# Kernel optimization log

Measured on AMD Instinct MI355X. Metric: run time of the kernel, lower is better.

The kernel has to match this reference:

```python
import jax, jax.numpy as jnp
import numpy as np

B, N, F, H, M, EF, OUT = 256, 32, 40, 100, 100, 4, 128
MESSAGE_PASSES = 3


def setup_inputs() -> dict:
    key = jax.random.key(0)
    ks = jax.random.split(key, 8)
    # Deterministic ring graphs: node i <-> node (i+1)%N, one-hot bond type.
    # Every node has degree 2 -> static nonzero counts.
    rng = np.random.default_rng(0)
    edges = np.zeros((B, N, N, EF), np.float32)
    b = np.arange(B)[:, None]
    i = np.arange(N)[None, :]
    j = (i + 1) % N
    t = rng.integers(0, EF, size=(B, N))
    edges[b, i, j, t] = 1.0
    edges[b, j, i, t] = 1.0

    nodes = jax.random.normal(ks[0], (B, N, F), jnp.float32)

    def init(k, shape, fan):
        return jax.random.normal(k, shape, jnp.float32) / np.sqrt(fan).astype(np.float32)

    W_msg = init(ks[1], (M, H, EF), H)          # MNN edge-conditioned weights
    W_ih = init(ks[2], (3 * H, M), M)            # GRUCell input weights
    W_hh = init(ks[3], (3 * H, H), H)            # GRUCell hidden weights
    b_ih = jnp.zeros((3 * H,), jnp.float32)
    b_hh = jnp.zeros((3 * H,), jnp.float32)
    Wg = init(ks[4], (H + F, H), H + F)          # gather gate
    bg = jnp.zeros((H,), jnp.float32)
    We = init(ks[5], (H, H), H)                  # gather embed
    be = jnp.zeros((H,), jnp.float32)
    Wo = init(ks[6], (H, OUT), H)                # output head
    bo = jnp.zeros((OUT,), jnp.float32)

    return {
        "nodes": nodes, "edges": jnp.asarray(edges),
        "W_msg": W_msg, "W_ih": W_ih, "W_hh": W_hh, "b_ih": b_ih, "b_hh": b_hh,
        "Wg": Wg, "bg": bg, "We": We, "be": be, "Wo": Wo, "bo": bo,
        "n_edges": B * N * 2, "n_node_entries": B * N,
    }


def gru_cell(x, h, W_ih, W_hh, b_ih, b_hh):
    gi = x @ W_ih.T + b_ih
    gh = h @ W_hh.T + b_hh
    ir, iz, inn = jnp.split(gi, 3, axis=-1)
    hr, hz, hn = jnp.split(gh, 3, axis=-1)
    r = jax.nn.sigmoid(ir + hr)
    z = jax.nn.sigmoid(iz + hz)
    n = jnp.tanh(inn + r * hn)
    return (1.0 - z) * n + z * h


def reference(nodes, edges, W_msg, W_ih, W_hh, b_ih, b_hh, Wg, bg, We, be, Wo, bo,
              n_edges, n_node_entries):
    adjacency = jnp.sum(edges, axis=3)                      # (B, N, N)
    eb, en, eg = jnp.nonzero(adjacency, size=n_edges)       # edge-level indices
    nb, nn_ = jnp.nonzero(adjacency.sum(-1), size=n_node_entries)

    # Dense one-hot segment-sum matrix: (n_node_entries, n_edges)
    same = (nb[:, None] == eb) & (nn_[:, None] == en)
    msg_sum_mat = same.astype(jnp.float32)

    edge_batch_edges = edges[eb, en, eg, :]                 # (E, EF)

    hidden = jnp.zeros((B, N, H), jnp.float32).at[:, :, :F].set(nodes)
    node_h = hidden[nb, nn_, :]                             # (V, H)

    for _ in range(MESSAGE_PASSES):
        nghb_h = hidden[eb, eg, :]                          # (E, H)
        # MNN message: sum_f edges[e,f] * W_msg[m,h,f] * nghb[e,h]
        message_terms = jnp.einsum('ef,mhf,eh->em', edge_batch_edges, W_msg, nghb_h)
        messages = msg_sum_mat @ message_terms              # (V, M) dense one-hot matmul
        node_h = gru_cell(messages, node_h, W_ih, W_hh, b_ih, b_hh)
        hidden = hidden.at[nb, nn_, :].set(node_h)

    node_mask = (adjacency.sum(-1) != 0).astype(jnp.float32)  # (B, N)
    cat = jnp.concatenate([hidden, nodes], axis=-1)           # (B, N, H+F)
    gate = jax.nn.sigmoid(cat @ Wg + bg)
    emb = gate * (hidden @ We + be)
    graph_emb = jnp.sum(emb * node_mask[..., None], axis=1)   # (B, H)
    return graph_emb @ Wo + bo                                # (B, OUT)
```

## Files before the change

### kernel.cpp

```cpp
#include <hip/hip_runtime.h>
#include <cstddef>
#include <cstdint>

#define B_   256
#define N_   32
#define F_   40
#define H_   100
#define OUT_ 128
#define CAP_ 8
#define TB   1024
#define XCS  168
#define XMS  136
#define NBLK 343
#define NLO  63

using bf16x8 = __attribute__((ext_vector_type(8))) short;
using f32x4  = __attribute__((ext_vector_type(4))) float;

__device__ __forceinline__ float sigmoidf_(float x){ return 1.0f/(1.0f+__expf(-x)); }
__device__ __forceinline__ float bf2f(short s){ return __uint_as_float(((uint32_t)(uint16_t)s)<<16); }
__device__ __forceinline__ short f2bf(float x){
  uint32_t u = __float_as_uint(x);
  return (short)((u + 0x7FFFu + ((u>>16)&1u))>>16);
}
__device__ __forceinline__ void bsplit(float x, short& hi, short& lo){
  hi = f2bf(x);
  lo = f2bf(x - bf2f(hi));
}

__global__ void prep_frags2(const float* __restrict__ Wmsg,
                            const float* __restrict__ Wih,
                            const float* __restrict__ Whh,
                            const float* __restrict__ Wg,
                            const float* __restrict__ We,
                            short* __restrict__ AFhi,
                            short* __restrict__ AFlo){
  int i = blockIdx.x*blockDim.x + threadIdx.x;
  if (i < 40000){
    float v = Wmsg[i];
    int t = i&3, mk = i>>2, h = mk%100, m = mk/100;
    int blk = t*28 + (m>>4)*4 + (h>>5);
    int lane = (m&15) + (((h&31)>>3)<<4);
    AFhi[(size_t)blk*512 + lane*8 + (h&7)] = f2bf(v);
  } else if (i < 70000){
    int i2 = i-40000;
    float v = Wih[i2];
    int jrow = i2/100, k = i2%100, mat = jrow/100, mg = jrow%100;
    int blk = 112 + mat*28 + (mg>>4)*4 + (k>>5);
    int lane = (mg&15) + (((k&31)>>3)<<4);
    AFhi[(size_t)blk*512 + lane*8 + (k&7)] = f2bf(v);
  } else if (i < 100000){
    int i2 = i-70000;
    float v = Whh[i2];
    int jrow = i2/100, k = i2%100, mat = 3 + jrow/100, mg = jrow%100;
    int blk = 112 + mat*28 + (mg>>4)*4 + (k>>5);
    int lane = (mg&15) + (((k&31)>>3)<<4);
    AFhi[(size_t)blk*512 + lane*8 + (k&7)] = f2bf(v);
  } else if (i < 114000){
    int i2 = i-100000;
    float v = Wg[i2];
    int k = i2/100, j = i2%100;
    int blk = 280 + (j>>4)*5 + (k>>5);
    int lane = (j&15) + (((k&31)>>3)<<4);
    short hi,lo; bsplit(v,hi,lo);
    AFhi[(size_t)blk*512 + lane*8 + (k&7)] = hi;
    AFlo[(size_t)(blk-280)*512 + lane*8 + (k&7)] = lo;
  } else if (i < 124000){
    int i2 = i-114000;
    float v = We[i2];
    int k = i2/100, j = i2%100;
    int blk = 315 + (j>>4)*4 + (k>>5);
    int lane = (j&15) + (((k&31)>>3)<<4);
    short hi,lo; bsplit(v,hi,lo);
    AFhi[(size_t)blk*512 + lane*8 + (k&7)] = hi;
    AFlo[(size_t)(blk-280)*512 + lane*8 + (k&7)] = lo;
  }
}

__device__ __forceinline__ bf16x8 ldB(const short* X, int stride, int nt, int ks, int lane){
  int n = nt*16 + (lane&15);
  return *(const bf16x8*)&X[n*stride + ks*32 + (lane>>4)*8];
}
__device__ __forceinline__ bf16x8 ldA(const short* __restrict__ AF, int blk, int lane){
  return *(const bf16x8*)(AF + (size_t)blk*512 + lane*8);
}

__global__ __launch_bounds__(TB, 4) void mpnn_mfma(
    const float* __restrict__ nodes, const float* __restrict__ edges,
    const short* __restrict__ AFhi, const short* __restrict__ AFlo,
    const float* __restrict__ b_ih, const float* __restrict__ b_hh,
    const float* __restrict__ bg, const float* __restrict__ be,
    const float* __restrict__ Wo, const float* __restrict__ bo,
    float* __restrict__ out){
  const int b = blockIdx.x;
  const int tid = threadIdx.x;
  const int lane = tid & 63;
  const int w = tid >> 6;

  __shared__ short XcH[32*XCS], XcL[32*XCS];
  __shared__ short XmH[32*XMS];
  __shared__ short XyH[4][32*XMS];
  __shared__ float sh_ge[H_];
  __shared__ float sh_part[4][OUT_];
  __shared__ float sh_rowsum[N_];
  __shared__ int   sh_cnt[N_];
  __shared__ int   sh_gt[N_][CAP_];
  __shared__ float sh_w[N_][CAP_];

  for (int i=tid;i<(32*XCS)/2;i+=TB){ ((int*)XcH)[i]=0; ((int*)XcL)[i]=0; }
  for (int i=tid;i<(32*XMS)/2;i+=TB){ ((int*)XmH)[i]=0; }
  if (tid < H_) sh_ge[tid]=0.0f;
  if (tid < N_){ sh_cnt[tid]=0; sh_rowsum[tid]=0.0f; }
  __syncthreads();

  for (int p=tid; p<N_*N_; p+=TB){
    int n = p>>5, g = p&31;
    const float4 ev = *(const float4*)(edges + (((size_t)b*N_+n)*N_+g)*4);
    float adj = ev.x+ev.y+ev.z+ev.w;
    if (adj != 0.0f){
      atomicAdd(&sh_rowsum[n], adj);
      float ef[4] = {ev.x,ev.y,ev.z,ev.w};
      for (int f=0; f<4; ++f)
        if (ef[f] != 0.0f){
          int s = atomicAdd(&sh_cnt[n],1);
          if (s<CAP_){ sh_gt[n][s]=(g<<2)|f; sh_w[n][s]=ef[f]; }
        }
    }
  }
  for (int p=tid; p<N_*F_; p+=TB){
    int n = p/F_, f = p%F_;
    float x = nodes[((size_t)b*N_+n)*F_ + f];
    short hi,lo; bsplit(x,hi,lo);
    XcH[n*XCS+f]=hi;      XcL[n*XCS+f]=lo;
    XcH[n*XCS+100+f]=hi;  XcL[n*XCS+100+f]=lo;
  }
  __syncthreads();

  const int jmt = w>>1, nt = w&1;
  const bool task = (w < 14);

  for (int pass=0; pass<3; ++pass){
    for (int it=0; it<2; ++it){
      int idx = tid + it*TB;
      int n = idx >> 6;
      int kp = idx & 63;
      int cnt = sh_cnt[n] < CAP_ ? sh_cnt[n] : CAP_;
      float s0[4]={0,0,0,0}, s1[4]={0,0,0,0};
      for (int e=0;e<cnt;++e){
        int gt = sh_gt[n][e];
        int g = gt>>2; float wv = sh_w[n][e];
        int hh = ((const int*)(XcH + g*XCS))[kp];
        float h0 = bf2f((short)(hh&0xffff));
        float h1 = bf2f((short)(hh>>16));
        int t = gt&3;
        if (t==0)      { s0[0]+=wv*h0; s1[0]+=wv*h1; }
        else if (t==1) { s0[1]+=wv*h0; s1[1]+=wv*h1; }
        else if (t==2) { s0[2]+=wv*h0; s1[2]+=wv*h1; }
        else           { s0[3]+=wv*h0; s1[3]+=wv*h1; }
      }
#pragma unroll
      for (int t=0;t<4;++t){
        ((int*)(XyH[t] + n*XMS))[kp] =
          (int)((uint16_t)f2bf(s0[t]) | ((uint32_t)(uint16_t)f2bf(s1[t])<<16));
      }
    }
    __syncthreads();
    f32x4 Ch0=(f32x4)0.0f, Ch1=(f32x4)0.0f, Ch2=(f32x4)0.0f;
    if (task){
      f32x4 Cm0=(f32x4)0.0f, Cm1=(f32x4)0.0f;
      {
        bf16x8 ah = ldA(AFhi, jmt*4, lane);
        bf16x8 bh = ldB(XyH[0],XMS,nt,0,lane);
#pragma unroll 1
        for (int i=0;i<16;++i){
          int ip = (i<15)? i+1 : 15;
          int tp = ip>>2, ksp = ip&3;
          bf16x8 an  = ldA(AFhi, tp*28+jmt*4+ksp, lane);
          bf16x8 bhn = ldB(XyH[tp],XMS,nt,ksp,lane);
          if (i<8) Cm0 = __builtin_amdgcn_mfma_f32_16x16x32_bf16(ah, bh, Cm0, 0,0,0);
          else     Cm1 = __builtin_amdgcn_mfma_f32_16x16x32_bf16(ah, bh, Cm1, 0,0,0);
          ah = an; bh = bhn;
        }
      }
      {
        bf16x8 ah = ldA(AFhi, 112+3*28+jmt*4, lane);
        bf16x8 bh = ldB(XcH,XCS,nt,0,lane);
#pragma unroll 1
        for (int i=0;i<12;++i){
          int ip = (i<11)? i+1 : 11;
          int gp = ip>>2, ksp = ip&3;
          bf16x8 an  = ldA(AFhi, 112+(gp+3)*28+jmt*4+ksp, lane);
          bf16x8 bhn = ldB(XcH,XCS,nt,ksp,lane);
          int g = i>>2;
          if (g==0)      Ch0 = __builtin_amdgcn_mfma_f32_16x16x32_bf16(ah, bh, Ch0, 0,0,0);
          else if (g==1) Ch1 = __builtin_amdgcn_mfma_f32_16x16x32_bf16(ah, bh, Ch1, 0,0,0);
          else           Ch2 = __builtin_amdgcn_mfma_f32_16x16x32_bf16(ah, bh, Ch2, 0,0,0);
          ah = an; bh = bhn;
        }
      }
      f32x4 Cm = Cm0 + Cm1;
      int n = nt*16+(lane&15);
      for (int r=0;r<4;++r){
        int row = jmt*16 + (lane>>4)*4 + r;
        if (row<100) XmH[n*XMS+row] = f2bf(Cm[r]);
      }
    }
    __syncthreads();
    if (task){
      f32x4 Ci0=(f32x4)0.0f, Ci1=(f32x4)0.0f, Ci2=(f32x4)0.0f;
      {
        bf16x8 ah = ldA(AFhi, 112+jmt*4, lane);
        bf16x8 bh = ldB(XmH,XMS,nt,0,lane);
#pragma unroll 1
        for (int i=0;i<12;++i){
          int ip = (i<11)? i+1 : 11;
          int gp = ip>>2, ksp = ip&3;
          bf16x8 an  = ldA(AFhi, 112+gp*28+jmt*4+ksp, lane);
          bf16x8 bhn = ldB(XmH,XMS,nt,ksp,lane);
          int g = i>>2;
          if (g==0)      Ci0 = __builtin_amdgcn_mfma_f32_16x16x32_bf16(ah, bh, Ci0, 0,0,0);
          else if (g==1) Ci1 = __builtin_amdgcn_mfma_f32_16x16x32_bf16(ah, bh, Ci1, 0,0,0);
          else           Ci2 = __builtin_amdgcn_mfma_f32_16x16x32_bf16(ah, bh, Ci2, 0,0,0);
          ah = an; bh = bhn;
        }
      }
      int n = nt*16+(lane&15);
      bool msk = (sh_rowsum[n] != 0.0f);
      for (int r=0;r<4;++r){
        int row = jmt*16 + (lane>>4)*4 + r;
        if (row<100){
          float ho = bf2f(XcH[n*XCS+row]) + bf2f(XcL[n*XCS+row]);
          float rr = sigmoidf_(Ci0[r]+Ch0[r] + b_ih[row]     + b_hh[row]);
          float zz = sigmoidf_(Ci1[r]+Ch1[r] + b_ih[100+row] + b_hh[100+row]);
          float nn = tanhf(Ci2[r] + b_ih[200+row] + rr*(Ch2[r] + b_hh[200+row]));
          float hnew = (1.0f-zz)*nn + zz*ho;
          if (!msk) hnew = ho;
          short hi,lo; bsplit(hnew,hi,lo);
          XcH[n*XCS+row]=hi; XcL[n*XCS+row]=lo;
        }
      }
    }
    __syncthreads();
  }

  f32x4 Cg=(f32x4)0.0f, Ce=(f32x4)0.0f;
  if (task){
    bf16x8 ah = ldA(AFhi, 280+jmt*5, lane);
    bf16x8 al = ldA(AFlo, jmt*5, lane);
    bf16x8 bh = ldB(XcH,XCS,nt,0,lane);
#pragma unroll 1
    for (int i=0;i<9;++i){
      int ip = (i<8)? i+1 : 8;
      int blkp  = (ip<5)? 280+jmt*5+ip : 315+jmt*4+(ip-5);
      int ksp   = (ip<5)? ip : ip-5;
      bf16x8 an  = ldA(AFhi, blkp, lane);
      bf16x8 aln = ldA(AFlo, blkp-280, lane);
      bf16x8 bhn = ldB(XcH,XCS,nt,ksp,lane);
      if (i<5){
        Cg = __builtin_amdgcn_mfma_f32_16x16x32_bf16(ah, bh, Cg, 0,0,0);
        Cg = __builtin_amdgcn_mfma_f32_16x16x32_bf16(al, bh, Cg, 0,0,0);
      } else {
        Ce = __builtin_amdgcn_mfma_f32_16x16x32_bf16(ah, bh, Ce, 0,0,0);
        Ce = __builtin_amdgcn_mfma_f32_16x16x32_bf16(al, bh, Ce, 0,0,0);
      }
      ah = an; al = aln; bh = bhn;
    }
    int n = nt*16+(lane&15);
    bool msk = (sh_rowsum[n] != 0.0f);
    for (int r=0;r<4;++r){
      int row = jmt*16 + (lane>>4)*4 + r;
      float v = 0.0f;
      if (row<100){
        float gate = sigmoidf_(Cg[r] + bg[row]);
        float emb  = gate*(Ce[r] + be[row]);
        v = msk ? emb : 0.0f;
      }
      v += __shfl_xor(v, 1);
      v += __shfl_xor(v, 2);
      v += __shfl_xor(v, 4);
      v += __shfl_xor(v, 8);
      if (row<100 && (lane&15)==0) atomicAdd(&sh_ge[row], v);
    }
  }
  __syncthreads();
  if (tid < 512){
    int o = tid & 127, q = tid >> 7;
    float s = 0.0f;
    int k0 = 25*q;
#pragma unroll 5
    for (int k=k0; k<k0+25; ++k) s += sh_ge[k]*Wo[k*OUT_+o];
    sh_part[q][o] = s;
  }
  __syncthreads();
  if (tid < OUT_){
    out[(size_t)b*OUT_ + tid] = bo[tid] + sh_part[0][tid] + sh_part[1][tid]
                              + sh_part[2][tid] + sh_part[3][tid];
  }
}

extern "C" void kernel_launch(void* const* d_in, const int* in_sizes, int n_in,
                              void* d_out, int out_size, void* d_ws, size_t ws_size,
                              hipStream_t stream){
  const float* nodes = (const float*)d_in[0];
  const float* edges = (const float*)d_in[1];
  const float* W_msg = (const float*)d_in[2];
  const float* W_ih  = (const float*)d_in[3];
  const float* W_hh  = (const float*)d_in[4];
  const float* b_ih  = (const float*)d_in[5];
  const float* b_hh  = (const float*)d_in[6];
  const float* Wg    = (const float*)d_in[7];
  const float* bg    = (const float*)d_in[8];
  const float* We    = (const float*)d_in[9];
  const float* be    = (const float*)d_in[10];
  const float* Wo    = (const float*)d_in[11];
  const float* bo    = (const float*)d_in[12];

  short* AFhi = (short*)d_ws;
  short* AFlo = AFhi + (size_t)NBLK*512;
  size_t af_bytes = ((size_t)NBLK + NLO) * 512 * sizeof(short);

  hipMemsetAsync(d_ws, 0, af_bytes, stream);
  prep_frags2<<<(124000 + 255)/256, 256, 0, stream>>>(W_msg, W_ih, W_hh, Wg, We,
                                                      AFhi, AFlo);
  mpnn_mfma<<<B_, TB, 0, stream>>>(nodes, edges, AFhi, AFlo, b_ih, b_hh, bg, be,
                                   Wo, bo, (float*)d_out);
}
```

Measured before the change: 133.9 us.

## Fold message weights into GRU input weights and use MFMA for neighbor aggregation

Precomputes W_ih·W_msg per edge type in the prep kernel, so the message matmul and the GRU input matmul collapse into one 48-step MFMA chain. This removes one stage and one barrier per pass. Neighbor aggregation moves from a per-edge list loop to a dense adjacency-by-hidden MFMA over a transposed hidden copy. The hidden state is double-buffered, tanh uses a fast exp form, and the memset is dropped because the prep kernel now writes every slot. In exchange it does more MFMA work on the dense 32x32 adjacency, and folding the weights changes where bf16 rounding happens.

New measurement: 153.9 us. 15.0% more time.

```diff
diff --git a/kernel.cpp b/kernel.cpp
--- a/kernel.cpp
+++ b/kernel.cpp
@@ -7,17 +7,21 @@
 #define F_   40
 #define H_   100
 #define OUT_ 128
-#define CAP_ 8
 #define TB   1024
 #define XCS  168
 #define XMS  136
-#define NBLK 343
+#define ST2  40
+#define NBLK 483
 #define NLO  63
 
 using bf16x8 = __attribute__((ext_vector_type(8))) short;
 using f32x4  = __attribute__((ext_vector_type(4))) float;
 
 __device__ __forceinline__ float sigmoidf_(float x){ return 1.0f/(1.0f+__expf(-x)); }
+__device__ __forceinline__ float tanhf_(float x){
+  float e = __expf(2.0f*x);
+  return 1.0f - 2.0f/(e+1.0f);
+}
 __device__ __forceinline__ float bf2f(short s){ return __uint_as_float(((uint32_t)(uint16_t)s)<<16); }
 __device__ __forceinline__ short f2bf(float x){
   uint32_t u = __float_as_uint(x);
@@ -28,52 +32,48 @@
   lo = f2bf(x - bf2f(hi));
 }
 
-__global__ void prep_frags2(const float* __restrict__ Wmsg,
+__global__ void prep_frags3(const float* __restrict__ Wmsg,
                             const float* __restrict__ Wih,
                             const float* __restrict__ Whh,
                             const float* __restrict__ Wg,
                             const float* __restrict__ We,
                             short* __restrict__ AFhi,
                             short* __restrict__ AFlo){
-  int i = blockIdx.x*blockDim.x + threadIdx.x;
-  if (i < 40000){
-    float v = Wmsg[i];
-    int t = i&3, mk = i>>2, h = mk%100, m = mk/100;
-    int blk = t*28 + (m>>4)*4 + (h>>5);
-    int lane = (m&15) + (((h&31)>>3)<<4);
-    AFhi[(size_t)blk*512 + lane*8 + (h&7)] = f2bf(v);
-  } else if (i < 70000){
-    int i2 = i-40000;
-    float v = Wih[i2];
-    int jrow = i2/100, k = i2%100, mat = jrow/100, mg = jrow%100;
-    int blk = 112 + mat*28 + (mg>>4)*4 + (k>>5);
-    int lane = (mg&15) + (((k&31)>>3)<<4);
-    AFhi[(size_t)blk*512 + lane*8 + (k&7)] = f2bf(v);
-  } else if (i < 100000){
-    int i2 = i-70000;
-    float v = Whh[i2];
-    int jrow = i2/100, k = i2%100, mat = 3 + jrow/100, mg = jrow%100;
-    int blk = 112 + mat*28 + (mg>>4)*4 + (k>>5);
-    int lane = (mg&15) + (((k&31)>>3)<<4);
-    AFhi[(size_t)blk*512 + lane*8 + (k&7)] = f2bf(v);
-  } else if (i < 114000){
-    int i2 = i-100000;
-    float v = Wg[i2];
-    int k = i2/100, j = i2%100;
-    int blk = 280 + (j>>4)*5 + (k>>5);
-    int lane = (j&15) + (((k&31)>>3)<<4);
+  int slot = blockIdx.x*blockDim.x + threadIdx.x;
+  if (slot >= NBLK*512) return;
+  int blk = slot>>9, r = slot&511, lane = r>>3, jj = r&7;
+  int m = lane&15, q = lane>>4, kl = q*8+jj;
+  if (blk < 336){
+    int sub = blk/28, rem = blk%28;
+    int g = sub>>2, t = sub&3, jmt = rem>>2, ks = rem&3;
+    int jo = jmt*16+m, h = ks*32+kl;
+    float v = 0.0f;
+    if (jo<100 && h<100){
+      const float* wr = Wih + (g*100+jo)*100;
+      const float* wc = Wmsg + h*4 + t;
+#pragma unroll 4
+      for (int m2=0;m2<100;++m2) v += wr[m2]*wc[m2*400];
+    }
+    AFhi[slot] = f2bf(v);
+  } else if (blk < 420){
+    int bb = blk-336, mat = bb/28, rem = bb%28, jmt = rem>>2, ks = rem&3;
+    int jo = jmt*16+m, k = ks*32+kl;
+    float v = (jo<100 && k<100) ? Whh[(mat*100+jo)*100+k] : 0.0f;
+    AFhi[slot] = f2bf(v);
+  } else if (blk < 455){
+    int bb = blk-420, jmt = bb/5, ks = bb%5;
+    int jo = jmt*16+m, k = ks*32+kl;
+    float v = (jo<100 && k<140) ? Wg[k*100+jo] : 0.0f;
     short hi,lo; bsplit(v,hi,lo);
-    AFhi[(size_t)blk*512 + lane*8 + (k&7)] = hi;
-    AFlo[(size_t)(blk-280)*512 + lane*8 + (k&7)] = lo;
-  } else if (i < 124000){
-    int i2 = i-114000;
-    float v = We[i2];
-    int k = i2/100, j = i2%100;
-    int blk = 315 + (j>>4)*4 + (k>>5);
-    int lane = (j&15) + (((k&31)>>3)<<4);
+    AFhi[slot] = hi;
+    AFlo[(size_t)(blk-420)*512 + lane*8 + jj] = lo;
+  } else {
+    int bb = blk-455, jmt = bb>>2, ks = bb&3;
+    int jo = jmt*16+m, k = ks*32+kl;
+    float v = (jo<100 && k<100) ? We[k*100+jo] : 0.0f;
     short hi,lo; bsplit(v,hi,lo);
-    AFhi[(size_t)blk*512 + lane*8 + (k&7)] = hi;
-    AFlo[(size_t)(blk-280)*512 + lane*8 + (k&7)] = lo;
+    AFhi[slot] = hi;
+    AFlo[(size_t)(blk-420)*512 + lane*8 + jj] = lo;
   }
 }
 
@@ -97,100 +97,94 @@
   const int lane = tid & 63;
   const int w = tid >> 6;
 
-  __shared__ short XcH[32*XCS], XcL[32*XCS];
-  __shared__ short XmH[32*XMS];
-  __shared__ short XyH[4][32*XMS];
+  __shared__ short XcH[2][32*XCS];
+  __shared__ short XcL[32*XCS];
+  __shared__ short XcT[2][112*ST2];
+  __shared__ short XyH[4*32*XMS];
+  __shared__ short Aw[4*32*32];
   __shared__ float sh_ge[H_];
   __shared__ float sh_part[4][OUT_];
   __shared__ float sh_rowsum[N_];
-  __shared__ int   sh_cnt[N_];
-  __shared__ int   sh_gt[N_][CAP_];
-  __shared__ float sh_w[N_][CAP_];
-
-  for (int i=tid;i<(32*XCS)/2;i+=TB){ ((int*)XcH)[i]=0; ((int*)XcL)[i]=0; }
-  for (int i=tid;i<(32*XMS)/2;i+=TB){ ((int*)XmH)[i]=0; }
+
+  for (int i=tid;i<32*XCS;i+=TB){ XcH[0][i]=0; XcH[1][i]=0; XcL[i]=0; }
+  for (int i=tid;i<2*112*ST2;i+=TB){ ((short*)XcT)[i]=0; }
+  for (int i=tid;i<4*32*XMS;i+=TB){ XyH[i]=0; }
+  for (int i=tid;i<4*32*32;i+=TB){ Aw[i]=0; }
   if (tid < H_) sh_ge[tid]=0.0f;
-  if (tid < N_){ sh_cnt[tid]=0; sh_rowsum[tid]=0.0f; }
-  __syncthreads();
-
-  for (int p=tid; p<N_*N_; p+=TB){
-    int n = p>>5, g = p&31;
+  if (tid < N_) sh_rowsum[tid]=0.0f;
+  __syncthreads();
+
+  {
+    int n = tid>>5, g = tid&31;
     const float4 ev = *(const float4*)(edges + (((size_t)b*N_+n)*N_+g)*4);
     float adj = ev.x+ev.y+ev.z+ev.w;
     if (adj != 0.0f){
       atomicAdd(&sh_rowsum[n], adj);
       float ef[4] = {ev.x,ev.y,ev.z,ev.w};
       for (int f=0; f<4; ++f)
-        if (ef[f] != 0.0f){
-          int s = atomicAdd(&sh_cnt[n],1);
-          if (s<CAP_){ sh_gt[n][s]=(g<<2)|f; sh_w[n][s]=ef[f]; }
-        }
+        if (ef[f] != 0.0f) Aw[f*1024 + n*32 + g] = f2bf(ef[f]);
     }
   }
   for (int p=tid; p<N_*F_; p+=TB){
     int n = p/F_, f = p%F_;
     float x = nodes[((size_t)b*N_+n)*F_ + f];
     short hi,lo; bsplit(x,hi,lo);
-    XcH[n*XCS+f]=hi;      XcL[n*XCS+f]=lo;
-    XcH[n*XCS+100+f]=hi;  XcL[n*XCS+100+f]=lo;
+    XcH[0][n*XCS+f]=hi;       XcL[n*XCS+f]=lo;
+    XcH[0][n*XCS+100+f]=hi;   XcH[1][n*XCS+100+f]=hi;
+    XcT[0][f*ST2+n]=hi;
   }
   __syncthreads();
 
   const int jmt = w>>1, nt = w&1;
   const bool task = (w < 14);
+  int cur = 0;
 
   for (int pass=0; pass<3; ++pass){
-    for (int it=0; it<2; ++it){
-      int idx = tid + it*TB;
-      int n = idx >> 6;
-      int kp = idx & 63;
-      int cnt = sh_cnt[n] < CAP_ ? sh_cnt[n] : CAP_;
-      float s0[4]={0,0,0,0}, s1[4]={0,0,0,0};
-      for (int e=0;e<cnt;++e){
-        int gt = sh_gt[n][e];
-        int g = gt>>2; float wv = sh_w[n][e];
-        int hh = ((const int*)(XcH + g*XCS))[kp];
-        float h0 = bf2f((short)(hh&0xffff));
-        float h1 = bf2f((short)(hh>>16));
-        int t = gt&3;
-        if (t==0)      { s0[0]+=wv*h0; s1[0]+=wv*h1; }
-        else if (t==1) { s0[1]+=wv*h0; s1[1]+=wv*h1; }
-        else if (t==2) { s0[2]+=wv*h0; s1[2]+=wv*h1; }
-        else           { s0[3]+=wv*h0; s1[3]+=wv*h1; }
-      }
+    const int nxt = cur^1;
+    if (task){
+      bf16x8 bfr = *(const bf16x8*)&XcT[cur][(jmt*16+(lane&15))*ST2 + (lane>>4)*8];
+      int kf = jmt*16 + (lane&15);
 #pragma unroll
       for (int t=0;t<4;++t){
-        ((int*)(XyH[t] + n*XMS))[kp] =
-          (int)((uint16_t)f2bf(s0[t]) | ((uint32_t)(uint16_t)f2bf(s1[t])<<16));
+        bf16x8 af = *(const bf16x8*)&Aw[t*1024 + (nt*16+(lane&15))*32 + (lane>>4)*8];
+        f32x4 D = (f32x4)0.0f;
+        D = __builtin_amdgcn_mfma_f32_16x16x32_bf16(af, bfr, D, 0,0,0);
+        if (kf < 100){
+#pragma unroll
+          for (int r=0;r<4;++r)
+            XyH[t*32*XMS + (nt*16+(lane>>4)*4+r)*XMS + kf] = f2bf(D[r]);
+        }
       }
     }
     __syncthreads();
-    f32x4 Ch0=(f32x4)0.0f, Ch1=(f32x4)0.0f, Ch2=(f32x4)0.0f;
     if (task){
-      f32x4 Cm0=(f32x4)0.0f, Cm1=(f32x4)0.0f;
+      f32x4 Cg0=(f32x4)0.0f, Cg1=(f32x4)0.0f, Cg2=(f32x4)0.0f;
       {
         bf16x8 ah = ldA(AFhi, jmt*4, lane);
-        bf16x8 bh = ldB(XyH[0],XMS,nt,0,lane);
+        bf16x8 bh = ldB(XyH, XMS, nt, 0, lane);
 #pragma unroll 1
-        for (int i=0;i<16;++i){
-          int ip = (i<15)? i+1 : 15;
-          int tp = ip>>2, ksp = ip&3;
-          bf16x8 an  = ldA(AFhi, tp*28+jmt*4+ksp, lane);
-          bf16x8 bhn = ldB(XyH[tp],XMS,nt,ksp,lane);
-          if (i<8) Cm0 = __builtin_amdgcn_mfma_f32_16x16x32_bf16(ah, bh, Cm0, 0,0,0);
-          else     Cm1 = __builtin_amdgcn_mfma_f32_16x16x32_bf16(ah, bh, Cm1, 0,0,0);
+        for (int i=0;i<48;++i){
+          int ip = (i<47)? i+1 : 47;
+          int gp = ip>>4, tp = (ip>>2)&3, ksp = ip&3;
+          bf16x8 an  = ldA(AFhi, (gp*4+tp)*28 + jmt*4 + ksp, lane);
+          bf16x8 bhn = ldB(XyH + tp*32*XMS, XMS, nt, ksp, lane);
+          int g = i>>4;
+          if (g==0)      Cg0 = __builtin_amdgcn_mfma_f32_16x16x32_bf16(ah, bh, Cg0, 0,0,0);
+          else if (g==1) Cg1 = __builtin_amdgcn_mfma_f32_16x16x32_bf16(ah, bh, Cg1, 0,0,0);
+          else           Cg2 = __builtin_amdgcn_mfma_f32_16x16x32_bf16(ah, bh, Cg2, 0,0,0);
           ah = an; bh = bhn;
         }
       }
+      f32x4 Ch0=(f32x4)0.0f, Ch1=(f32x4)0.0f, Ch2=(f32x4)0.0f;
       {
-        bf16x8 ah = ldA(AFhi, 112+3*28+jmt*4, lane);
-        bf16x8 bh = ldB(XcH,XCS,nt,0,lane);
+        bf16x8 ah = ldA(AFhi, 336 + jmt*4, lane);
+        bf16x8 bh = ldB(XcH[cur], XCS, nt, 0, lane);
 #pragma unroll 1
         for (int i=0;i<12;++i){
           int ip = (i<11)? i+1 : 11;
-          int gp = ip>>2, ksp = ip&3;
-          bf16x8 an  = ldA(AFhi, 112+(gp+3)*28+jmt*4+ksp, lane);
-          bf16x8 bhn = ldB(XcH,XCS,nt,ksp,lane);
+          int mp = ip>>2, ksp = ip&3;
+          bf16x8 an  = ldA(AFhi, 336 + mp*28 + jmt*4 + ksp, lane);
+          bf16x8 bhn = ldB(XcH[cur], XCS, nt, ksp, lane);
           int g = i>>2;
           if (g==0)      Ch0 = __builtin_amdgcn_mfma_f32_16x16x32_bf16(ah, bh, Ch0, 0,0,0);
           else if (g==1) Ch1 = __builtin_amdgcn_mfma_f32_16x16x32_bf16(ah, bh, Ch1, 0,0,0);
@@ -198,64 +192,40 @@
           ah = an; bh = bhn;
         }
       }
-      f32x4 Cm = Cm0 + Cm1;
-      int n = nt*16+(lane&15);
-      for (int r=0;r<4;++r){
-        int row = jmt*16 + (lane>>4)*4 + r;
-        if (row<100) XmH[n*XMS+row] = f2bf(Cm[r]);
-      }
-    }
-    __syncthreads();
-    if (task){
-      f32x4 Ci0=(f32x4)0.0f, Ci1=(f32x4)0.0f, Ci2=(f32x4)0.0f;
-      {
-        bf16x8 ah = ldA(AFhi, 112+jmt*4, lane);
-        bf16x8 bh = ldB(XmH,XMS,nt,0,lane);
-#pragma unroll 1
-        for (int i=0;i<12;++i){
-          int ip = (i<11)? i+1 : 11;
-          int gp = ip>>2, ksp = ip&3;
-          bf16x8 an  = ldA(AFhi, 112+gp*28+jmt*4+ksp, lane);
-          bf16x8 bhn = ldB(XmH,XMS,nt,ksp,lane);
-          int g = i>>2;
-          if (g==0)      Ci0 = __builtin_amdgcn_mfma_f32_16x16x32_bf16(ah, bh, Ci0, 0,0,0);
-          else if (g==1) Ci1 = __builtin_amdgcn_mfma_f32_16x16x32_bf16(ah, bh, Ci1, 0,0,0);
-          else           Ci2 = __builtin_amdgcn_mfma_f32_16x16x32_bf16(ah, bh, Ci2, 0,0,0);
-          ah = an; bh = bhn;
-        }
-      }
       int n = nt*16+(lane&15);
       bool msk = (sh_rowsum[n] != 0.0f);
+#pragma unroll
       for (int r=0;r<4;++r){
         int row = jmt*16 + (lane>>4)*4 + r;
         if (row<100){
-          float ho = bf2f(XcH[n*XCS+row]) + bf2f(XcL[n*XCS+row]);
-          float rr = sigmoidf_(Ci0[r]+Ch0[r] + b_ih[row]     + b_hh[row]);
-          float zz = sigmoidf_(Ci1[r]+Ch1[r] + b_ih[100+row] + b_hh[100+row]);
-          float nn = tanhf(Ci2[r] + b_ih[200+row] + rr*(Ch2[r] + b_hh[200+row]));
+          float ho = bf2f(XcH[cur][n*XCS+row]) + bf2f(XcL[n*XCS+row]);
+          float rr = sigmoidf_(Cg0[r]+Ch0[r] + b_ih[row]     + b_hh[row]);
+          float zz = sigmoidf_(Cg1[r]+Ch1[r] + b_ih[100+row] + b_hh[100+row]);
+          float nn = tanhf_(Cg2[r] + b_ih[200+row] + rr*(Ch2[r] + b_hh[200+row]));
           float hnew = (1.0f-zz)*nn + zz*ho;
           if (!msk) hnew = ho;
           short hi,lo; bsplit(hnew,hi,lo);
-          XcH[n*XCS+row]=hi; XcL[n*XCS+row]=lo;
+          XcH[nxt][n*XCS+row]=hi; XcL[n*XCS+row]=lo; XcT[nxt][row*ST2+n]=hi;
         }
       }
     }
     __syncthreads();
+    cur ^= 1;
   }
 
   f32x4 Cg=(f32x4)0.0f, Ce=(f32x4)0.0f;
   if (task){
-    bf16x8 ah = ldA(AFhi, 280+jmt*5, lane);
+    bf16x8 ah = ldA(AFhi, 420+jmt*5, lane);
     bf16x8 al = ldA(AFlo, jmt*5, lane);
-    bf16x8 bh = ldB(XcH,XCS,nt,0,lane);
+    bf16x8 bh = ldB(XcH[cur], XCS, nt, 0, lane);
 #pragma unroll 1
     for (int i=0;i<9;++i){
       int ip = (i<8)? i+1 : 8;
-      int blkp  = (ip<5)? 280+jmt*5+ip : 315+jmt*4+(ip-5);
-      int ksp   = (ip<5)? ip : ip-5;
+      int blkp = (ip<5)? 420+jmt*5+ip : 455+jmt*4+(ip-5);
+      int ksp  = (ip<5)? ip : ip-5;
       bf16x8 an  = ldA(AFhi, blkp, lane);
-      bf16x8 aln = ldA(AFlo, blkp-280, lane);
-      bf16x8 bhn = ldB(XcH,XCS,nt,ksp,lane);
+      bf16x8 aln = ldA(AFlo, blkp-420, lane);
+      bf16x8 bhn = ldB(XcH[cur], XCS, nt, ksp, lane);
       if (i<5){
         Cg = __builtin_amdgcn_mfma_f32_16x16x32_bf16(ah, bh, Cg, 0,0,0);
         Cg = __builtin_amdgcn_mfma_f32_16x16x32_bf16(al, bh, Cg, 0,0,0);
@@ -267,6 +237,7 @@
     }
     int n = nt*16+(lane&15);
     bool msk = (sh_rowsum[n] != 0.0f);
+#pragma unroll
     for (int r=0;r<4;++r){
       int row = jmt*16 + (lane>>4)*4 + r;
       float v = 0.0f;
@@ -317,11 +288,9 @@
 
   short* AFhi = (short*)d_ws;
   short* AFlo = AFhi + (size_t)NBLK*512;
-  size_t af_bytes = ((size_t)NBLK + NLO) * 512 * sizeof(short);
-
-  hipMemsetAsync(d_ws, 0, af_bytes, stream);
-  prep_frags2<<<(124000 + 255)/256, 256, 0, stream>>>(W_msg, W_ih, W_hh, Wg, We,
-                                                      AFhi, AFlo);
+
+  prep_frags3<<<(NBLK*512 + 255)/256, 256, 0, stream>>>(W_msg, W_ih, W_hh, Wg, We,
+                                                        AFhi, AFlo);
   mpnn_mfma<<<B_, TB, 0, stream>>>(nodes, edges, AFhi, AFlo, b_ih, b_hh, bg, be,
                                    Wo, bo, (float*)d_out);
 }
```
